# Kernel tuning notes

Hardware: AMD Instinct MI355X
Metric: run time of the kernel (lower is better)

The kernel has to match this reference:

```python
import jax, jax.numpy as jnp
import numpy as np

EPS = 0.1        # entropic regularization epsilon
MAX_ITER = 15    # fixed number of Sinkhorn iterations (no early stop for determinism)
TINY = 1e-16     # denominator stabilizer, matches torch code
NORM_EPS = 1e-8  # cosine-norm clamp, matches torch code


def setup_inputs() -> dict:
    key = jax.random.key(0)
    k1, k2 = jax.random.split(key)
    x = jax.random.normal(k1, (32, 512, 256), dtype=jnp.float32)
    y = jax.random.normal(k2, (32, 512, 256), dtype=jnp.float32)
    return {"x": x, "y": y}


def _cosine_distance(x, y):
    # C[b,n,m] = 1 - <x_n, y_m> / max(|x_n||y_m|, eps)
    w1 = jnp.linalg.norm(x, axis=-1, keepdims=True)            # [b,n,1]
    w2 = jnp.linalg.norm(y, axis=-1, keepdims=True)            # [b,m,1]
    dots = jnp.einsum('bnd,bmd->bnm', x, y)                    # [b,n,m]
    denom = jnp.maximum(w1 * jnp.swapaxes(w2, -2, -1), NORM_EPS)
    return 1.0 - dots / denom


def _sinkhorn(C):
    nb, n, m = C.shape
    # uniform marginals (a=None, b=None in the torch module); mask is all ones
    a = jnp.full((nb, n), 1.0 / n, dtype=C.dtype)
    b = jnp.full((nb, m), 1.0 / m, dtype=C.dtype)

    def log_K(alpha, beta):
        # log K = (-C + alpha 1^T + 1 beta^T) / eps
        return (-C + alpha[:, :, None] + beta[:, None, :]) / EPS

    def step(carry, _):
        u, v, alpha, beta = carry
        K = jnp.exp(log_K(alpha, beta))
        u = a / (jnp.einsum('bnm,bm->bn', K, v) + TINY)   # K v
        v = b / (jnp.einsum('bnm,bn->bm', K, u) + TINY)   # K^T u
        alpha = alpha + EPS * jnp.log(u)  # absorb u into log scaling
        beta = beta + EPS * jnp.log(v)    # absorb v into log scaling
        return (u, v, alpha, beta), None

    init = (jnp.ones((nb, n), C.dtype), jnp.ones((nb, m), C.dtype),
            jnp.zeros((nb, n), C.dtype), jnp.zeros((nb, m), C.dtype))
    (u, v, alpha, beta), _ = jax.lax.scan(step, init, None, length=MAX_ITER)

    # P = exp(log u + log K + log v) with the FINAL alpha/beta (as in torch code)
    pi = jnp.exp(jnp.log(u)[:, :, None] + log_K(alpha, beta) + jnp.log(v)[:, None, :])
    cost = jnp.sum(pi * C, axis=(-2, -1))  # reduction='none' -> per-batch cost [nb]
    return cost, pi, C


def reference(x, y):
    C = _cosine_distance(x, y)
    return _sinkhorn(C)
```

## Files before the change

### kernel.cpp

```cpp
#include <hip/hip_runtime.h>
#include <hip/hip_fp16.h>
#include <math.h>

#define NB 32
#define NN 512
#define DD 256
#define NROW  (NB*NN)
#define NELEM (NB*NN*DD)

constexpr float INV_EPS   = 10.0f;
constexpr float F_TINY    = 1e-16f;
constexpr float F_NORMEPS = 1e-8f;
constexpr float MARG      = 1.0f / 512.0f;

typedef __attribute__((ext_vector_type(8))) short bf16x8;
typedef __attribute__((ext_vector_type(4))) float f32x4;

__device__ __forceinline__ unsigned short f2bf(float f) {
    unsigned u = __float_as_uint(f);
    u += 0x7fffu + ((u >> 16) & 1u);
    return (unsigned short)(u >> 16);
}

__global__ __launch_bounds__(256) void norms_convert(
        const float* __restrict__ x, const float* __restrict__ y,
        float* __restrict__ nx, float* __restrict__ ny,
        unsigned short* __restrict__ xh, unsigned short* __restrict__ yh,
        float* __restrict__ cost) {
    if (blockIdx.x == 0 && threadIdx.x < NB) cost[threadIdx.x] = 0.0f;
    int w = threadIdx.x >> 6, l = threadIdx.x & 63;
    int row = blockIdx.x * 4 + w;
    bool isx = row < NROW;
    int r = isx ? row : row - NROW;
    const float* src = (isx ? x : y) + (size_t)r * DD;
    float4 v = ((const float4*)src)[l];
    float ss = v.x * v.x + v.y * v.y + v.z * v.z + v.w * v.w;
#pragma unroll
    for (int off = 32; off; off >>= 1) ss += __shfl_xor(ss, off);

    unsigned short* ph = (isx ? xh : yh) + (size_t)r * DD + l * 4;
    *(ushort4*)ph = make_ushort4(f2bf(v.x), f2bf(v.y), f2bf(v.z), f2bf(v.w));
    if (l == 0) (isx ? nx : ny)[r] = sqrtf(ss);
}

__global__ __launch_bounds__(256) void gemm_cos_mfma(
        const unsigned short* __restrict__ xh, const unsigned short* __restrict__ yh,
        const float* __restrict__ nx, const float* __restrict__ ny,
        float* __restrict__ C, __half* __restrict__ Ef) {
    int blk = blockIdx.x;
    int b = blk >> 4, ti = (blk >> 2) & 3, tj = blk & 3;
    __shared__ short Ah[128][32], Bh[128][32];
    const unsigned short* xbh = xh + ((size_t)b * NN + ti * 128) * DD;
    const unsigned short* ybh = yh + ((size_t)b * NN + tj * 128) * DD;
    int t = threadIdx.x, w = t >> 6, l = t & 63;
    int rw = w * 32, q = l >> 4, low = l & 15;

    f32x4 acc[2][8];
#pragma unroll
    for (int i = 0; i < 2; ++i)
#pragma unroll
        for (int j = 0; j < 8; ++j) acc[i][j] = (f32x4){0.f, 0.f, 0.f, 0.f};

    int sr = t >> 1, h = t & 1;
    int c0i = 2 * h, c1i = 2 * h + 1;
    int sw0 = (c0i ^ ((sr >> 1) & 3)) * 8;
    int sw1 = (c1i ^ ((sr >> 1) & 3)) * 8;

    for (int k0 = 0; k0 < DD; k0 += 32) {
        {
            const int4* ga = (const int4*)(xbh + (size_t)sr * DD + k0);
            const int4* gc = (const int4*)(ybh + (size_t)sr * DD + k0);
            int4 a0 = ga[c0i], a1 = ga[c1i];
            int4 c0 = gc[c0i], c1 = gc[c1i];
            *(int4*)&Ah[sr][sw0] = a0; *(int4*)&Ah[sr][sw1] = a1;
            *(int4*)&Bh[sr][sw0] = c0; *(int4*)&Bh[sr][sw1] = c1;
        }
        __syncthreads();

        bf16x8 ah[2];
#pragma unroll
        for (int ti2 = 0; ti2 < 2; ++ti2) {
            int m = rw + ti2 * 16 + low;
            int pq = (q ^ ((m >> 1) & 3)) * 8;
            ah[ti2] = *(const bf16x8*)&Ah[m][pq];
        }
#pragma unroll
        for (int tj2 = 0; tj2 < 8; ++tj2) {
            int n = tj2 * 16 + low;
            int pq = (q ^ ((n >> 1) & 3)) * 8;
            bf16x8 bh = *(const bf16x8*)&Bh[n][pq];
#pragma unroll
            for (int ti2 = 0; ti2 < 2; ++ti2)
                acc[ti2][tj2] = __builtin_amdgcn_mfma_f32_16x16x32_bf16(
                    ah[ti2], bh, acc[ti2][tj2], 0, 0, 0);
        }
        __syncthreads();
    }

    float*  Cb = C  + (size_t)b * NN * NN;
    __half* Eb = Ef + (size_t)b * NN * NN;
#pragma unroll
    for (int ti2 = 0; ti2 < 2; ++ti2) {
#pragma unroll
        for (int tj2 = 0; tj2 < 8; ++tj2) {
            int gm0 = ti * 128 + rw + ti2 * 16 + q * 4;
            int gn  = tj * 128 + tj2 * 16 + low;
            float nyc = ny[b * NN + gn];
            f32x4 a = acc[ti2][tj2];
#pragma unroll
            for (int reg = 0; reg < 4; ++reg) {
                int gm = gm0 + reg;
                float d = 1.0f - a[reg] / fmaxf(nx[b * NN + gm] * nyc, F_NORMEPS);
                Cb[(size_t)gm * NN + gn] = d;
                Eb[(size_t)gm * NN + gn] = __float2half(__expf(-INV_EPS * d));
            }
        }
    }
}

__global__ __launch_bounds__(512) void sink_iter(
        const __half* __restrict__ Ef, const float* __restrict__ cp_prev,
        float* __restrict__ cp_cur, float* __restrict__ A_g,
        const float* __restrict__ B_rd, float* __restrict__ B_wr,
        float* __restrict__ P, int t) {
    int blk = blockIdx.x;
    int xcd = blk & 7, qq = blk >> 3;
    int o = qq & 7;
    int b = ((qq >> 3) << 3) | xcd;
    int blkbase = blk - 8 * o;
    int tt = threadIdx.x, w = tt >> 6, l = tt & 63;
    int r0 = o * 64 + w * 8;

    __shared__ float sW[NN];
    __shared__ float sWP[8][NN];

    if (t == 1) {
        sW[tt] = 1.0f;
    } else {
        float sv = 0.0f;
#pragma unroll
        for (int k = 0; k < 8; ++k)
            sv += cp_prev[(size_t)(blkbase + 8 * k) * NN + tt];
        float Bc = (t == 2) ? 1.0f : B_rd[b * NN + tt];
        float vv = MARG / (Bc * sv + F_TINY);
        float Bn = Bc * vv;
        sW[tt] = Bn * vv;
        if (o == 0) B_wr[b * NN + tt] = Bn;
    }

    float E[8][8];
    const __half* Eb = Ef + ((size_t)b * NN + r0) * NN + 8 * l;
#pragma unroll
    for (int i = 0; i < 8; ++i) {
        int4 raw = *(const int4*)(Eb + (size_t)i * NN);
        const __half* hv = (const __half*)&raw;
#pragma unroll
        for (int e = 0; e < 8; ++e) E[i][e] = __half2float(hv[e]);
    }
    float A[8];
#pragma unroll
    for (int i = 0; i < 8; ++i)
        A[i] = (t == 1) ? 1.0f : A_g[b * NN + r0 + i];
    __syncthreads();

    float wr[8];
    *(float4*)&wr[0] = *(const float4*)&sW[8 * l];
    *(float4*)&wr[4] = *(const float4*)&sW[8 * l + 4];
#pragma unroll
    for (int i = 0; i < 8; ++i) {
        float s = 0.0f;
#pragma unroll
        for (int e = 0; e < 8; ++e) s = fmaf(E[i][e], wr[e], s);
#pragma unroll
        for (int off = 32; off; off >>= 1) s += __shfl_xor(s, off);
        float uu = MARG / (A[i] * s + F_TINY);
        A[i] *= uu;
        if (l == 0) {
            if (t == 15) P[b * NN + r0 + i] = A[i] * uu;
            else         A_g[b * NN + r0 + i] = A[i];
        }
    }

    float p[8];
#pragma unroll
    for (int e = 0; e < 8; ++e) {
        float s = 0.0f;
#pragma unroll
        for (int i = 0; i < 8; ++i) s = fmaf(E[i][e], A[i], s);
        p[e] = s;
    }
    *(float4*)&sWP[w][8 * l]     = make_float4(p[0], p[1], p[2], p[3]);
    *(float4*)&sWP[w][8 * l + 4] = make_float4(p[4], p[5], p[6], p[7]);
    __syncthreads();
    float cs = 0.0f;
#pragma unroll
    for (int ww = 0; ww < 8; ++ww) cs += sWP[ww][tt];
    cp_cur[(size_t)blk * NN + tt] = cs;
}

__global__ __launch_bounds__(512) void finish_q(
        const float* __restrict__ cp, const float* __restrict__ B_rd,
        float* __restrict__ Q) {
    int b = blockIdx.x, tt = threadIdx.x;
    int blkbase = ((b >> 3) << 6) | (b & 7);
    float sv = 0.0f;
#pragma unroll
    for (int k = 0; k < 8; ++k)
        sv += cp[(size_t)(blkbase + 8 * k) * NN + tt];
    float Bc = B_rd[b * NN + tt];
    float vv = MARG / (Bc * sv + F_TINY);
    Q[b * NN + tt] = Bc * vv * vv;
}

__global__ __launch_bounds__(256) void pi_cost(
        const float* __restrict__ C, const float* __restrict__ P,
        const float* __restrict__ Q, float* __restrict__ pi,
        float* __restrict__ cost) {
    int b = blockIdx.x >> 4, rg = blockIdx.x & 15;
    __shared__ float sQ[NN];
    __shared__ float sPart[4];
    for (int i = threadIdx.x; i < NN; i += 256) sQ[i] = Q[b * NN + i];
    __syncthreads();
    int w = threadIdx.x >> 6, l = threadIdx.x & 63;
    float q0[8];
    *(float4*)&q0[0] = *(const float4*)&sQ[4 * l];
    *(float4*)&q0[4] = *(const float4*)&sQ[256 + 4 * l];
    const float* Cb = C + (size_t)b * NN * NN;
    float* pib = pi + (size_t)b * NN * NN;
    float csum = 0.0f;
#pragma unroll 1
    for (int i = 0; i < 8; ++i) {
        int r = rg * 32 + w * 8 + i;
        float pf = P[b * NN + r];
        const float* crow = Cb + (size_t)r * NN;
        float* prow = pib + (size_t)r * NN;
        float4 c0 = *(const float4*)(crow + 4 * l);
        float4 c1 = *(const float4*)(crow + 256 + 4 * l);
        float pv0 = pf * q0[0] * __expf(-INV_EPS * c0.x);
        float pv1 = pf * q0[1] * __expf(-INV_EPS * c0.y);
        float pv2 = pf * q0[2] * __expf(-INV_EPS * c0.z);
        float pv3 = pf * q0[3] * __expf(-INV_EPS * c0.w);
        float pv4 = pf * q0[4] * __expf(-INV_EPS * c1.x);
        float pv5 = pf * q0[5] * __expf(-INV_EPS * c1.y);
        float pv6 = pf * q0[6] * __expf(-INV_EPS * c1.z);
        float pv7 = pf * q0[7] * __expf(-INV_EPS * c1.w);
        *(float4*)(prow + 4 * l)       = make_float4(pv0, pv1, pv2, pv3);
        *(float4*)(prow + 256 + 4 * l) = make_float4(pv4, pv5, pv6, pv7);
        csum = fmaf(pv0, c0.x, csum); csum = fmaf(pv1, c0.y, csum);
        csum = fmaf(pv2, c0.z, csum); csum = fmaf(pv3, c0.w, csum);
        csum = fmaf(pv4, c1.x, csum); csum = fmaf(pv5, c1.y, csum);
        csum = fmaf(pv6, c1.z, csum); csum = fmaf(pv7, c1.w, csum);
    }
#pragma unroll
    for (int off = 32; off; off >>= 1) csum += __shfl_xor(csum, off);
    if (l == 0) sPart[w] = csum;
    __syncthreads();
    if (threadIdx.x == 0) {
        float tot = sPart[0] + sPart[1] + sPart[2] + sPart[3];
        atomicAdd(&cost[b], tot);
    }
}

extern "C" void kernel_launch(void* const* d_in, const int* in_sizes, int n_in,
                              void* d_out, int out_size, void* d_ws, size_t ws_size,
                              hipStream_t stream) {
    const float* x = (const float*)d_in[0];
    const float* y = (const float*)d_in[1];
    float* out  = (float*)d_out;
    float* cost = out;
    float* pi   = out + 32;
    float* C    = out + 32 + (size_t)NB * NN * NN;

    float* ws = (float*)d_ws;
    float* nx = ws;
    float* ny = ws + 16384;
    float* P  = ws + 32768;
    float* Q  = ws + 49152;
    float* A  = ws + 65536;
    float* Bb[2] = { ws + 81920, ws + 98304 };

    unsigned short* xh = (unsigned short*)pi;
    unsigned short* yh = xh + NELEM;
    __half* Ef = (__half*)(yh + NELEM);
    float* cp[2] = { pi, pi + 256 * NN };

    norms_convert<<<dim3(8192), dim3(256), 0, stream>>>(
        x, y, nx, ny, xh, yh, cost);
    gemm_cos_mfma<<<dim3(512), dim3(256), 0, stream>>>(
        xh, yh, nx, ny, C, Ef);

    for (int t = 1; t <= 15; ++t) {
        sink_iter<<<dim3(256), dim3(512), 0, stream>>>(
            Ef, cp[(t - 1) & 1], cp[t & 1], A,
            Bb[t & 1], Bb[(t - 1) & 1], P, t);
    }
    finish_q<<<dim3(32), dim3(512), 0, stream>>>(cp[1], Bb[0], Q);
    pi_cost<<<dim3(512), dim3(256), 0, stream>>>(C, P, Q, pi, cost);
}
```

Baseline: 205.6 us.

## Fuse Sinkhorn iterations and pi/cost into one cooperative persistent kernel

```diff
diff --git a/kernel.cpp b/kernel.cpp
--- a/kernel.cpp
+++ b/kernel.cpp
@@ -26,8 +26,9 @@
         const float* __restrict__ x, const float* __restrict__ y,
         float* __restrict__ nx, float* __restrict__ ny,
         unsigned short* __restrict__ xh, unsigned short* __restrict__ yh,
-        float* __restrict__ cost) {
+        float* __restrict__ cost, int* __restrict__ bars) {
     if (blockIdx.x == 0 && threadIdx.x < NB) cost[threadIdx.x] = 0.0f;
+    if (blockIdx.x == 0 && threadIdx.x < 33) bars[threadIdx.x] = 0;
     int w = threadIdx.x >> 6, l = threadIdx.x & 63;
     int row = blockIdx.x * 4 + w;
     bool isx = row < NROW;
@@ -118,11 +119,11 @@
     }
 }
 
-__global__ __launch_bounds__(512) void sink_iter(
-        const __half* __restrict__ Ef, const float* __restrict__ cp_prev,
-        float* __restrict__ cp_cur, float* __restrict__ A_g,
-        const float* __restrict__ B_rd, float* __restrict__ B_wr,
-        float* __restrict__ P, int t) {
+__global__ __launch_bounds__(512, 2) void sink_fused(
+        const __half* __restrict__ Ef, const float* __restrict__ C,
+        float* __restrict__ cp0, float* __restrict__ cp1,
+        float* __restrict__ pi, float* __restrict__ cost,
+        int* __restrict__ bars) {
     int blk = blockIdx.x;
     int xcd = blk & 7, qq = blk >> 3;
     int o = qq & 7;
@@ -133,20 +134,7 @@
 
     __shared__ float sW[NN];
     __shared__ float sWP[8][NN];
-
-    if (t == 1) {
-        sW[tt] = 1.0f;
-    } else {
-        float sv = 0.0f;
-#pragma unroll
-        for (int k = 0; k < 8; ++k)
-            sv += cp_prev[(size_t)(blkbase + 8 * k) * NN + tt];
-        float Bc = (t == 2) ? 1.0f : B_rd[b * NN + tt];
-        float vv = MARG / (Bc * sv + F_TINY);
-        float Bn = Bc * vv;
-        sW[tt] = Bn * vv;
-        if (o == 0) B_wr[b * NN + tt] = Bn;
-    }
+    __shared__ float sPart[8];
 
     float E[8][8];
     const __half* Eb = Ef + ((size_t)b * NN + r0) * NN + 8 * l;
@@ -157,81 +145,106 @@
 #pragma unroll
         for (int e = 0; e < 8; ++e) E[i][e] = __half2float(hv[e]);
     }
-    float A[8];
-#pragma unroll
-    for (int i = 0; i < 8; ++i)
-        A[i] = (t == 1) ? 1.0f : A_g[b * NN + r0 + i];
+
+    float A[8], Pr[8];
+#pragma unroll
+    for (int i = 0; i < 8; ++i) { A[i] = 1.0f; Pr[i] = 0.0f; }
+    float Br = 1.0f;
+
+    float* cpr = cp0;
+    float* cpw = cp1;
+
+    for (int t = 1; t <= 15; ++t) {
+        if (t == 1) {
+            sW[tt] = 1.0f;
+        } else {
+            float sv = 0.0f;
+#pragma unroll
+            for (int k = 0; k < 8; ++k)
+                sv += cpr[(size_t)(blkbase + 8 * k) * NN + tt];
+            float vv = MARG / (Br * sv + F_TINY);
+            Br *= vv;
+            sW[tt] = Br * vv;
+        }
+        __syncthreads();
+
+        float wr[8];
+        *(float4*)&wr[0] = *(const float4*)&sW[8 * l];
+        *(float4*)&wr[4] = *(const float4*)&sW[8 * l + 4];
+#pragma unroll
+        for (int i = 0; i < 8; ++i) {
+            float s = 0.0f;
+#pragma unroll
+            for (int e = 0; e < 8; ++e) s = fmaf(E[i][e], wr[e], s);
+#pragma unroll
+            for (int off = 32; off; off >>= 1) s += __shfl_xor(s, off);
+            float uu = MARG / (A[i] * s + F_TINY);
+            A[i] *= uu;
+            if (t == 15) Pr[i] = A[i] * uu;
+        }
+
+        float p[8];
+#pragma unroll
+        for (int e = 0; e < 8; ++e) {
+            float s = 0.0f;
+#pragma unroll
+            for (int i = 0; i < 8; ++i) s = fmaf(E[i][e], A[i], s);
+            p[e] = s;
+        }
+        *(float4*)&sWP[w][8 * l]     = make_float4(p[0], p[1], p[2], p[3]);
+        *(float4*)&sWP[w][8 * l + 4] = make_float4(p[4], p[5], p[6], p[7]);
+        __syncthreads();
+        float cs = 0.0f;
+#pragma unroll
+        for (int ww = 0; ww < 8; ++ww) cs += sWP[ww][tt];
+        cpw[(size_t)blk * NN + tt] = cs;
+
+        __syncthreads();
+        if (tt == 0) {
+            __threadfence();
+            __hip_atomic_fetch_add(&bars[b], 1, __ATOMIC_RELAXED,
+                                   __HIP_MEMORY_SCOPE_AGENT);
+            while (__hip_atomic_load(&bars[b], __ATOMIC_RELAXED,
+                                     __HIP_MEMORY_SCOPE_AGENT) < 8 * t)
+                __builtin_amdgcn_s_sleep(1);
+            __threadfence();
+        }
+        __syncthreads();
+
+        float* tmp = cpr; cpr = cpw; cpw = tmp;
+    }
+
+    {
+        float sv = 0.0f;
+#pragma unroll
+        for (int k = 0; k < 8; ++k)
+            sv += cpr[(size_t)(blkbase + 8 * k) * NN + tt];
+        float vv = MARG / (Br * sv + F_TINY);
+        sW[tt] = Br * vv * vv;
+    }
+
     __syncthreads();
-
-    float wr[8];
-    *(float4*)&wr[0] = *(const float4*)&sW[8 * l];
-    *(float4*)&wr[4] = *(const float4*)&sW[8 * l + 4];
-#pragma unroll
-    for (int i = 0; i < 8; ++i) {
-        float s = 0.0f;
-#pragma unroll
-        for (int e = 0; e < 8; ++e) s = fmaf(E[i][e], wr[e], s);
-#pragma unroll
-        for (int off = 32; off; off >>= 1) s += __shfl_xor(s, off);
-        float uu = MARG / (A[i] * s + F_TINY);
-        A[i] *= uu;
-        if (l == 0) {
-            if (t == 15) P[b * NN + r0 + i] = A[i] * uu;
-            else         A_g[b * NN + r0 + i] = A[i];
-        }
-    }
-
-    float p[8];
-#pragma unroll
-    for (int e = 0; e < 8; ++e) {
-        float s = 0.0f;
-#pragma unroll
-        for (int i = 0; i < 8; ++i) s = fmaf(E[i][e], A[i], s);
-        p[e] = s;
-    }
-    *(float4*)&sWP[w][8 * l]     = make_float4(p[0], p[1], p[2], p[3]);
-    *(float4*)&sWP[w][8 * l + 4] = make_float4(p[4], p[5], p[6], p[7]);
+    if (tt == 0) {
+        __threadfence();
+        __hip_atomic_fetch_add(&bars[32], 1, __ATOMIC_RELAXED,
+                               __HIP_MEMORY_SCOPE_AGENT);
+        while (__hip_atomic_load(&bars[32], __ATOMIC_RELAXED,
+                                 __HIP_MEMORY_SCOPE_AGENT) < 256)
+            __builtin_amdgcn_s_sleep(1);
+        __threadfence();
+    }
     __syncthreads();
-    float cs = 0.0f;
-#pragma unroll
-    for (int ww = 0; ww < 8; ++ww) cs += sWP[ww][tt];
-    cp_cur[(size_t)blk * NN + tt] = cs;
-}
-
-__global__ __launch_bounds__(512) void finish_q(
-        const float* __restrict__ cp, const float* __restrict__ B_rd,
-        float* __restrict__ Q) {
-    int b = blockIdx.x, tt = threadIdx.x;
-    int blkbase = ((b >> 3) << 6) | (b & 7);
-    float sv = 0.0f;
-#pragma unroll
-    for (int k = 0; k < 8; ++k)
-        sv += cp[(size_t)(blkbase + 8 * k) * NN + tt];
-    float Bc = B_rd[b * NN + tt];
-    float vv = MARG / (Bc * sv + F_TINY);
-    Q[b * NN + tt] = Bc * vv * vv;
-}
-
-__global__ __launch_bounds__(256) void pi_cost(
-        const float* __restrict__ C, const float* __restrict__ P,
-        const float* __restrict__ Q, float* __restrict__ pi,
-        float* __restrict__ cost) {
-    int b = blockIdx.x >> 4, rg = blockIdx.x & 15;
-    __shared__ float sQ[NN];
-    __shared__ float sPart[4];
-    for (int i = threadIdx.x; i < NN; i += 256) sQ[i] = Q[b * NN + i];
-    __syncthreads();
-    int w = threadIdx.x >> 6, l = threadIdx.x & 63;
+
     float q0[8];
-    *(float4*)&q0[0] = *(const float4*)&sQ[4 * l];
-    *(float4*)&q0[4] = *(const float4*)&sQ[256 + 4 * l];
+    *(float4*)&q0[0] = *(const float4*)&sW[4 * l];
+    *(float4*)&q0[4] = *(const float4*)&sW[256 + 4 * l];
     const float* Cb = C + (size_t)b * NN * NN;
     float* pib = pi + (size_t)b * NN * NN;
     float csum = 0.0f;
 #pragma unroll 1
     for (int i = 0; i < 8; ++i) {
-        int r = rg * 32 + w * 8 + i;
-        float pf = P[b * NN + r];
+        int r = o * 64 + w * 8 + i;
+        float pf = Pr[i];
         const float* crow = Cb + (size_t)r * NN;
         float* prow = pib + (size_t)r * NN;
         float4 c0 = *(const float4*)(crow + 4 * l);
@@ -255,8 +268,10 @@
     for (int off = 32; off; off >>= 1) csum += __shfl_xor(csum, off);
     if (l == 0) sPart[w] = csum;
     __syncthreads();
-    if (threadIdx.x == 0) {
-        float tot = sPart[0] + sPart[1] + sPart[2] + sPart[3];
+    if (tt == 0) {
+        float tot = 0.0f;
+#pragma unroll
+        for (int ww = 0; ww < 8; ++ww) tot += sPart[ww];
         atomicAdd(&cost[b], tot);
     }
 }
@@ -274,26 +289,23 @@
     float* ws = (float*)d_ws;
     float* nx = ws;
     float* ny = ws + 16384;
-    float* P  = ws + 32768;
-    float* Q  = ws + 49152;
-    float* A  = ws + 65536;
-    float* Bb[2] = { ws + 81920, ws + 98304 };
+    int* bars = (int*)(ws + 32768);
 
     unsigned short* xh = (unsigned short*)pi;
     unsigned short* yh = xh + NELEM;
     __half* Ef = (__half*)(yh + NELEM);
-    float* cp[2] = { pi, pi + 256 * NN };
+    float* cp0 = pi;
+    float* cp1 = pi + 256 * NN;
 
     norms_convert<<<dim3(8192), dim3(256), 0, stream>>>(
-        x, y, nx, ny, xh, yh, cost);
+        x, y, nx, ny, xh, yh, cost, bars);
     gemm_cos_mfma<<<dim3(512), dim3(256), 0, stream>>>(
         xh, yh, nx, ny, C, Ef);
 
-    for (int t = 1; t <= 15; ++t) {
-        sink_iter<<<dim3(256), dim3(512), 0, stream>>>(
-            Ef, cp[(t - 1) & 1], cp[t & 1], A,
-            Bb[t & 1], Bb[(t - 1) & 1], P, t);
-    }
-    finish_q<<<dim3(32), dim3(512), 0, stream>>>(cp[1], Bb[0], Q);
-    pi_cost<<<dim3(512), dim3(256), 0, stream>>>(C, P, Q, pi, cost);
-}
+    const __half* Ef_p = Ef; const float* C_p = C;
+    float* cp0_p = cp0; float* cp1_p = cp1;
+    float* pi_p = pi; float* cost_p = cost; int* bars_p = bars;
+    void* args[] = { &Ef_p, &C_p, &cp0_p, &cp1_p, &pi_p, &cost_p, &bars_p };
+    hipLaunchCooperativeKernel(reinterpret_cast<void*>(sink_fused),
+                               dim3(256), dim3(512), args, 0, stream);
+}
```

Result: slower. 434.7 us (+111.5%).
